# Optimization experiments

Hardware: AMD Instinct MI355X
Metric: run time of the kernel (lower is better)

Reference implementation:

```python
import jax, jax.numpy as jnp
import numpy as np

B, A, E = 8192, 56, 128          # batch, num_altas (=tgt_len), embed_dim
H, HD = 4, 16                     # num_heads, head_dim = E // H // 2
LAMBDA_INIT = 0.7
EPS = 1e-5
SCALING = HD ** -0.5


def _conv1d(x, w, b):
    # x: [N, C_in, L], w: [C_out, C_in, K], 'same' padding for K=7
    y = jax.lax.conv_general_dilated(
        x, w, window_strides=(1,), padding=[(3, 3)],
        dimension_numbers=('NCH', 'OIH', 'NCH'))
    return y + b[None, :, None]


def _layernorm(v, w, b):
    m = jnp.mean(v, axis=-1, keepdims=True)
    var = jnp.mean(jnp.square(v - m), axis=-1, keepdims=True)
    return (v - m) * jax.lax.rsqrt(var + EPS) * w + b


def setup_inputs() -> dict:
    key = jax.random.key(0)
    ks = jax.random.split(key, 12)
    return {
        'x': jax.random.normal(ks[0], (B, A, E), dtype=jnp.float32),
        'w_emb': jax.random.normal(ks[1], (A, A, 7), dtype=jnp.float32) * 0.05,
        'b_emb': jnp.zeros((A,), dtype=jnp.float32),
        'w_atlas': jax.random.normal(ks[2], (E, E, 7), dtype=jnp.float32) * 0.03,
        'b_atlas': jnp.zeros((E,), dtype=jnp.float32),
        'w_k': jax.random.normal(ks[3], (E, E), dtype=jnp.float32) * 0.08,
        'qn_w': jnp.ones((HD,), dtype=jnp.float32),
        'qn_b': jnp.zeros((HD,), dtype=jnp.float32),
        'kn_w': jnp.ones((HD,), dtype=jnp.float32),
        'kn_b': jnp.zeros((HD,), dtype=jnp.float32),
        'lambda_q1': jax.random.normal(ks[4], (HD,), dtype=jnp.float32) * 0.1,
        'lambda_k1': jax.random.normal(ks[5], (HD,), dtype=jnp.float32) * 0.1,
        'lambda_q2': jax.random.normal(ks[6], (HD,), dtype=jnp.float32) * 0.1,
        'lambda_k2': jax.random.normal(ks[7], (HD,), dtype=jnp.float32) * 0.1,
    }


def reference(x, w_emb, b_emb, w_atlas, b_atlas, w_k,
              qn_w, qn_b, kn_w, kn_b,
              lambda_q1, lambda_k1, lambda_q2, lambda_k2):
    bsz, tgt_len, embed_dim = x.shape
    # query formation: conv over atlas channels, SiLU, conv over embed channels,
    # SiLU, mean-pool over atlas positions -> [B, 1, E]
    h = jax.nn.silu(_conv1d(x, w_emb, b_emb))                  # [B, A, E]
    h = jax.nn.silu(_conv1d(h.transpose(0, 2, 1), w_atlas, b_atlas))  # [B, E, A]
    q = jnp.mean(h, axis=2)[:, None, :]                         # [B, 1, E]

    k = jnp.einsum('ble,oe->blo', x, w_k)                       # [B, A, E]

    q = q.reshape(bsz, 1, 2 * H, HD)
    k = k.reshape(bsz, tgt_len, 2 * H, HD)
    q = _layernorm(q, qn_w, qn_b) * SCALING
    k = _layernorm(k, kn_w, kn_b)

    attn = jnp.einsum('bqhe,bkhe->bhqk', q, k)                  # [B, 2H, 1, A]
    attn = jax.nn.softmax(attn, axis=-1)

    lam1 = jnp.exp(jnp.sum(lambda_q1 * lambda_k1))
    lam2 = jnp.exp(jnp.sum(lambda_q2 * lambda_k2))
    lambda_full = lam1 - lam2 + LAMBDA_INIT

    attn = attn.reshape(bsz, H, 2, 1, tgt_len)
    diff = attn[:, :, 0] - lambda_full * attn[:, :, 1]          # [B, H, 1, A]
    out = jax.nn.softmax(diff, axis=-1).mean(axis=1)            # [B, 1, A]
    return out.reshape(bsz, -1)                                 # [B, A]
```

## Files before the change

### kernel.cpp

```cpp
#include <hip/hip_runtime.h>
#include <math.h>

#define A_DIM 56
#define E_DIM 128

typedef short short8 __attribute__((ext_vector_type(8)));
typedef float floatx4 __attribute__((ext_vector_type(4)));

#define XT_HI_B 0
#define XT_LO_B 19296
#define H_HI_B  0
#define H_LO_B  16864
#define XR_HI_B 0
#define XR_LO_B 15232
#define KM_B    0
#define Q_B     33728
#define QN_B    34240
#define LG_B    34752
#define DP_B    36672
#define LAM_B   38592
#define SMEM_B  38608

#define QF   (Q_B/4)
#define QNF  (QN_B/4)
#define LGF  (LG_B/4)
#define DPF  (DP_B/4)
#define LAMF (LAM_B/4)
#define KP2  132

#define W1H 0
#define W1L 28672
#define W2H 57344
#define W2L 172032
#define WKH 286720
#define WKL 303104
#define PREP_ELEMS 159744

__device__ __forceinline__ unsigned rne16(unsigned u) {
  return (u + 0x7FFFu + ((u >> 16) & 1u)) >> 16;
}
__device__ __forceinline__ unsigned pack_hi16(unsigned u0, unsigned u1) {
  return __builtin_amdgcn_perm(u1, u0, 0x07060302u);
}
__device__ __forceinline__ float silu_f(float v) { return v / (1.f + __expf(-v)); }

__global__ void prep_weights(const float* __restrict__ w_emb,
                             const float* __restrict__ w_atlas,
                             const float* __restrict__ w_k,
                             unsigned short* __restrict__ ws) {
  int idx = blockIdx.x * 256 + threadIdx.x;
  if (idx >= PREP_ELEMS) return;
  float v; int dst_hi, dst_lo;
  if (idx < 28672) {
    int tap = idx >> 12, kc = (idx >> 11) & 1, nt = (idx >> 9) & 3;
    int lm = (idx >> 5) & 15, lkg = (idx >> 3) & 3, jj = idx & 7;
    int a = nt * 16 + lm, ci = kc * 32 + lkg * 8 + jj;
    v = (a < A_DIM && ci < A_DIM) ? w_emb[(a * A_DIM + ci) * 7 + tap] : 0.f;
    dst_hi = W1H + idx; dst_lo = W1L + idx;
  } else if (idx < 143360) {
    int j = idx - 28672;
    int tap = j >> 14, kc = (j >> 12) & 3, mt = (j >> 9) & 7;
    int lm = (j >> 5) & 15, lkg = (j >> 3) & 3, jj = j & 7;
    int eo = mt * 16 + lm, ei = kc * 32 + lkg * 8 + jj;
    v = w_atlas[(eo * E_DIM + ei) * 7 + tap];
    dst_hi = W2H + j; dst_lo = W2L + j;
  } else {
    int j = idx - 143360;
    int kc = j >> 12, mt = (j >> 9) & 7;
    int lm = (j >> 5) & 15, lkg = (j >> 3) & 3, jj = j & 7;
    int o = mt * 16 + lm, e = kc * 32 + lkg * 8 + jj;
    v = w_k[o * E_DIM + e];
    dst_hi = WKH + j; dst_lo = WKL + j;
  }
  unsigned u = __float_as_uint(v);
  unsigned hi = rne16(u);
  float lof = v - __uint_as_float(hi << 16);
  unsigned lo = rne16(__float_as_uint(lof));
  ws[dst_hi] = (unsigned short)hi;
  ws[dst_lo] = (unsigned short)lo;
}

__global__ __launch_bounds__(256, 4)
void atlas_fused(const float* __restrict__ x,
                 const unsigned short* __restrict__ ws,
                 const float* __restrict__ b_emb, const float* __restrict__ b_atlas,
                 const float* __restrict__ qn_w,  const float* __restrict__ qn_b,
                 const float* __restrict__ kn_w,  const float* __restrict__ kn_b,
                 const float* __restrict__ lq1,   const float* __restrict__ lk1,
                 const float* __restrict__ lq2,   const float* __restrict__ lk2,
                 float* __restrict__ out)
{
  __shared__ __align__(16) unsigned char smem[SMEM_B];
  float* smf = (float*)smem;
  const int t = threadIdx.x;
  const int b = blockIdx.x;
  const int lane = t & 63;
  const int w = __builtin_amdgcn_readfirstlane(t >> 6);
  const int lm = lane & 15;
  const int lkg8 = (lane >> 4) * 8;
  const int lr = (lane >> 4) * 4;

  const float* xb = x + (size_t)b * (A_DIM * E_DIM);

  {
    uint4 z4 = make_uint4(0, 0, 0, 0);
    for (int i = t; i < 352; i += 256) {
      if (i < 268) {
        int arr = i & 1, row = i >> 1;
        *(uint4*)(smem + (arr ? XT_LO_B : XT_HI_B) + row * 144 + 112) = z4;
      } else {
        int j = i - 268;
        int arr = j / 42; j -= arr * 42;
        int rowi = j / 7, c = j - rowi * 7;
        int row = (rowi < 3) ? rowi : 128 + rowi;
        *(uint4*)(smem + (arr ? XT_LO_B : XT_HI_B) + row * 144 + c * 16) = z4;
      }
    }
    if (t == 0) {
      float s1 = 0.f, s2 = 0.f;
      for (int i = 0; i < 16; ++i) { s1 += lq1[i] * lk1[i]; s2 += lq2[i] * lk2[i]; }
      smf[LAMF] = expf(s1) - expf(s2) + 0.7f;
    }
    int ab = t & 15;
    if (ab < 14) {
#pragma unroll
      for (int p = 0; p < 2; ++p) {
        int eb = (t >> 4) + 16 * p;
        floatx4 r0 = *(const floatx4*)(xb + (4 * ab + 0) * 128 + 4 * eb);
        floatx4 r1 = *(const floatx4*)(xb + (4 * ab + 1) * 128 + 4 * eb);
        floatx4 r2 = *(const floatx4*)(xb + (4 * ab + 2) * 128 + 4 * eb);
        floatx4 r3 = *(const floatx4*)(xb + (4 * ab + 3) * 128 + 4 * eb);
#pragma unroll
        for (int j2 = 0; j2 < 4; ++j2) {
          unsigned u0 = __float_as_uint(r0[j2]);
          unsigned u1 = __float_as_uint(r1[j2]);
          unsigned u2 = __float_as_uint(r2[j2]);
          unsigned u3 = __float_as_uint(r3[j2]);
          float l0 = r0[j2] - __uint_as_float(u0 & 0xFFFF0000u);
          float l1 = r1[j2] - __uint_as_float(u1 & 0xFFFF0000u);
          float l2 = r2[j2] - __uint_as_float(u2 & 0xFFFF0000u);
          float l3 = r3[j2] - __uint_as_float(u3 & 0xFFFF0000u);
          int off = (4 * eb + j2 + 3) * 144 + 8 * ab;
          *(uint2*)(smem + XT_HI_B + off) =
              make_uint2(pack_hi16(u0, u1), pack_hi16(u2, u3));
          *(uint2*)(smem + XT_LO_B + off) =
              make_uint2(pack_hi16(__float_as_uint(l0), __float_as_uint(l1)),
                         pack_hi16(__float_as_uint(l2), __float_as_uint(l3)));
        }
      }
    }
  }
  __syncthreads();

  {
    floatx4 acc[2][4];
#pragma unroll
    for (int nt = 0; nt < 4; ++nt) {
      int a = nt * 16 + lm;
      float be = (a < A_DIM) ? b_emb[a] : 0.f;
#pragma unroll
      for (int mt = 0; mt < 2; ++mt) {
        acc[mt][nt][0] = be; acc[mt][nt][1] = be;
        acc[mt][nt][2] = be; acc[mt][nt][3] = be;
      }
    }
    const unsigned short* xh = (const unsigned short*)(smem + XT_HI_B);
    const unsigned short* xl = (const unsigned short*)(smem + XT_LO_B);
#pragma unroll 1
    for (int tap = 0; tap < 7; ++tap) {
      int arow0 = (32 * w + lm + tap) * 72;
      int arow1 = arow0 + 16 * 72;
#pragma unroll
      for (int kc = 0; kc < 2; ++kc) {
        int ko = kc * 32 + lkg8;
        const unsigned short* fb = ws + ((tap * 2 + kc) * 4) * 512 + lm * 32 + lkg8;
        short8 bh0 = *(const short8*)(fb + W1H);
        short8 bh1 = *(const short8*)(fb + W1H + 512);
        short8 bh2 = *(const short8*)(fb + W1H + 1024);
        short8 bh3 = *(const short8*)(fb + W1H + 1536);
        short8 bl0 = *(const short8*)(fb + W1L);
        short8 bl1 = *(const short8*)(fb + W1L + 512);
        short8 bl2 = *(const short8*)(fb + W1L + 1024);
        short8 bl3 = *(const short8*)(fb + W1L + 1536);
        short8 ah0 = *(const short8*)(xh + arow0 + ko);
        short8 ah1 = *(const short8*)(xh + arow1 + ko);
        short8 al0 = *(const short8*)(xl + arow0 + ko);
        short8 al1 = *(const short8*)(xl + arow1 + ko);
        short8 bh[4] = {bh0, bh1, bh2, bh3};
        short8 bl[4] = {bl0, bl1, bl2, bl3};
#pragma unroll
        for (int nt = 0; nt < 4; ++nt) {
          acc[0][nt] = __builtin_amdgcn_mfma_f32_16x16x32_bf16(ah0, bh[nt], acc[0][nt], 0, 0, 0);
          acc[0][nt] = __builtin_amdgcn_mfma_f32_16x16x32_bf16(al0, bh[nt], acc[0][nt], 0, 0, 0);
          acc[0][nt] = __builtin_amdgcn_mfma_f32_16x16x32_bf16(ah0, bl[nt], acc[0][nt], 0, 0, 0);
          acc[1][nt] = __builtin_amdgcn_mfma_f32_16x16x32_bf16(ah1, bh[nt], acc[1][nt], 0, 0, 0);
          acc[1][nt] = __builtin_amdgcn_mfma_f32_16x16x32_bf16(al1, bh[nt], acc[1][nt], 0, 0, 0);
          acc[1][nt] = __builtin_amdgcn_mfma_f32_16x16x32_bf16(ah1, bl[nt], acc[1][nt], 0, 0, 0);
        }
      }
    }
    __syncthreads();
    {
      uint4 z4 = make_uint4(0, 0, 0, 0);
      for (int i = t; i < 204; i += 256) {
        int arr = i / 102, j = i - arr * 102;
        int r6 = j / 17, c = j - r6 * 17;
        int row = (r6 < 3) ? r6 : 56 + r6;
        *(uint4*)(smem + (arr ? H_LO_B : H_HI_B) + row * 272 + c * 16) = z4;
      }
    }
#pragma unroll
    for (int mt = 0; mt < 2; ++mt) {
      int e0 = 16 * (2 * w + mt) + lr;
#pragma unroll
      for (int nt = 0; nt < 4; ++nt) {
        int a = 16 * nt + lm;
        if (a < A_DIM) {
          float v0 = silu_f(acc[mt][nt][0]), v1 = silu_f(acc[mt][nt][1]);
          float v2 = silu_f(acc[mt][nt][2]), v3 = silu_f(acc[mt][nt][3]);
          unsigned u0 = __float_as_uint(v0), u1 = __float_as_uint(v1);
          unsigned u2 = __float_as_uint(v2), u3 = __float_as_uint(v3);
          float l0 = v0 - __uint_as_float(u0 & 0xFFFF0000u);
          float l1 = v1 - __uint_as_float(u1 & 0xFFFF0000u);
          float l2 = v2 - __uint_as_float(u2 & 0xFFFF0000u);
          float l3 = v3 - __uint_as_float(u3 & 0xFFFF0000u);
          int off = (a + 3) * 272 + e0 * 2;
          *(uint2*)(smem + H_HI_B + off) = make_uint2(pack_hi16(u0, u1), pack_hi16(u2, u3));
          *(uint2*)(smem + H_LO_B + off) =
              make_uint2(pack_hi16(__float_as_uint(l0), __float_as_uint(l1)),
                         pack_hi16(__float_as_uint(l2), __float_as_uint(l3)));
        }
      }
    }
  }
  __syncthreads();

  {
    floatx4 acc[2][4];
#pragma unroll
    for (int mt = 0; mt < 2; ++mt) {
      int eo0 = 16 * (2 * w + mt) + lr;
      float c0 = b_atlas[eo0], c1 = b_atlas[eo0 + 1];
      float c2 = b_atlas[eo0 + 2], c3 = b_atlas[eo0 + 3];
#pragma unroll
      for (int nt = 0; nt < 4; ++nt) {
        acc[mt][nt][0] = c0; acc[mt][nt][1] = c1;
        acc[mt][nt][2] = c2; acc[mt][nt][3] = c3;
      }
    }
    const unsigned char* hh = smem + H_HI_B;
    const unsigned char* hl = smem + H_LO_B;
#pragma unroll 1
    for (int tap = 0; tap < 7; ++tap) {
      int rofs[4];
#pragma unroll
      for (int nt = 0; nt < 4; ++nt) {
        int r = 16 * nt + lm + tap;
        rofs[nt] = ((r > 61) ? 61 : r) * 272;
      }
#pragma unroll
      for (int kc = 0; kc < 4; ++kc) {
        int kob = (kc * 32 + lkg8) * 2;
        const unsigned short* fb = ws + ((tap * 4 + kc) * 8 + 2 * w) * 512 + lm * 32 + lkg8;
        short8 ah0 = *(const short8*)(fb + W2H);
        short8 ah1 = *(const short8*)(fb + W2H + 512);
        short8 al0 = *(const short8*)(fb + W2L);
        short8 al1 = *(const short8*)(fb + W2L + 512);
        short8 bh[4], bl[4];
#pragma unroll
        for (int nt = 0; nt < 4; ++nt) {
          bh[nt] = *(const short8*)(hh + rofs[nt] + kob);
          bl[nt] = *(const short8*)(hl + rofs[nt] + kob);
        }
#pragma unroll
        for (int nt = 0; nt < 4; ++nt) {
          acc[0][nt] = __builtin_amdgcn_mfma_f32_16x16x32_bf16(ah0, bh[nt], acc[0][nt], 0, 0, 0);
          acc[0][nt] = __builtin_amdgcn_mfma_f32_16x16x32_bf16(al0, bh[nt], acc[0][nt], 0, 0, 0);
          acc[0][nt] = __builtin_amdgcn_mfma_f32_16x16x32_bf16(ah0, bl[nt], acc[0][nt], 0, 0, 0);
          acc[1][nt] = __builtin_amdgcn_mfma_f32_16x16x32_bf16(ah1, bh[nt], acc[1][nt], 0, 0, 0);
          acc[1][nt] = __builtin_amdgcn_mfma_f32_16x16x32_bf16(al1, bh[nt], acc[1][nt], 0, 0, 0);
          acc[1][nt] = __builtin_amdgcn_mfma_f32_16x16x32_bf16(ah1, bl[nt], acc[1][nt], 0, 0, 0);
        }
      }
    }
#pragma unroll
    for (int mt = 0; mt < 2; ++mt) {
#pragma unroll
      for (int r = 0; r < 4; ++r) {
        float s = 0.f;
#pragma unroll
        for (int nt = 0; nt < 4; ++nt) {
          float v = silu_f(acc[mt][nt][r]);
          int a = 16 * nt + lm;
          s += (a < A_DIM) ? v : 0.f;
        }
        s += __shfl_xor(s, 1, 64);
        s += __shfl_xor(s, 2, 64);
        s += __shfl_xor(s, 4, 64);
        s += __shfl_xor(s, 8, 64);
        if (lm == 0) {
          int eo = 16 * (2 * w + mt) + lr + r;
          smf[QF + eo] = s * (1.f / 56.f);
        }
      }
    }
  }
  __syncthreads();

  if (t < 128) {
    float v = smf[QF + t];
    float s = v;
#pragma unroll
    for (int m = 1; m < 16; m <<= 1) s += __shfl_xor(s, m, 64);
    float mean = s * (1.f / 16.f);
    float d = v - mean;
    float s2 = d * d;
#pragma unroll
    for (int m = 1; m < 16; m <<= 1) s2 += __shfl_xor(s2, m, 64);
    float var = s2 * (1.f / 16.f);
    int dd = t & 15;
    float qn = d * rsqrtf(var + 1e-5f) * qn_w[dd] + qn_b[dd];
    smf[QNF + t] = qn * 0.25f;
  }
  for (int i = t; i < 1792; i += 256) {
    int a = i >> 5, e4 = i & 31;
    float4 v = *(const float4*)(xb + a * 128 + e4 * 4);
    unsigned u0 = __float_as_uint(v.x), u1 = __float_as_uint(v.y);
    unsigned u2 = __float_as_uint(v.z), u3 = __float_as_uint(v.w);
    float l0 = v.x - __uint_as_float(u0 & 0xFFFF0000u);
    float l1 = v.y - __uint_as_float(u1 & 0xFFFF0000u);
    float l2 = v.z - __uint_as_float(u2 & 0xFFFF0000u);
    float l3 = v.w - __uint_as_float(u3 & 0xFFFF0000u);
    int off = a * 272 + e4 * 8;
    *(uint2*)(smem + XR_HI_B + off) = make_uint2(pack_hi16(u0, u1), pack_hi16(u2, u3));
    *(uint2*)(smem + XR_LO_B + off) =
        make_uint2(pack_hi16(__float_as_uint(l0), __float_as_uint(l1)),
                   pack_hi16(__float_as_uint(l2), __float_as_uint(l3)));
  }
  __syncthreads();

  {
    floatx4 acc[2][4];
#pragma unroll
    for (int mt = 0; mt < 2; ++mt)
#pragma unroll
      for (int nt = 0; nt < 4; ++nt) {
        acc[mt][nt][0] = 0.f; acc[mt][nt][1] = 0.f;
        acc[mt][nt][2] = 0.f; acc[mt][nt][3] = 0.f;
      }
    const unsigned char* xrh = smem + XR_HI_B;
    const unsigned char* xrl = smem + XR_LO_B;
    int rofs[4];
#pragma unroll
    for (int nt = 0; nt < 4; ++nt) {
      int a = 16 * nt + lm;
      rofs[nt] = ((a > 55) ? 55 : a) * 272;
    }
#pragma unroll 1
    for (int kc = 0; kc < 4; ++kc) {
      int kob = (kc * 32 + lkg8) * 2;
      const unsigned short* fb = ws + (kc * 8 + 2 * w) * 512 + lm * 32 + lkg8;
      short8 ah0 = *(const short8*)(fb + WKH);
      short8 ah1 = *(const short8*)(fb + WKH + 512);
      short8 al0 = *(const short8*)(fb + WKL);
      short8 al1 = *(const short8*)(fb + WKL + 512);
      short8 bh[4], bl[4];
#pragma unroll
      for (int nt = 0; nt < 4; ++nt) {
        bh[nt] = *(const short8*)(xrh + rofs[nt] + kob);
        bl[nt] = *(const short8*)(xrl + rofs[nt] + kob);
      }
#pragma unroll
      for (int nt = 0; nt < 4; ++nt) {
        acc[0][nt] = __builtin_amdgcn_mfma_f32_16x16x32_bf16(ah0, bh[nt], acc[0][nt], 0, 0, 0);
        acc[0][nt] = __builtin_amdgcn_mfma_f32_16x16x32_bf16(al0, bh[nt], acc[0][nt], 0, 0, 0);
        acc[0][nt] = __builtin_amdgcn_mfma_f32_16x16x32_bf16(ah0, bl[nt], acc[0][nt], 0, 0, 0);
        acc[1][nt] = __builtin_amdgcn_mfma_f32_16x16x32_bf16(ah1, bh[nt], acc[1][nt], 0, 0, 0);
        acc[1][nt] = __builtin_amdgcn_mfma_f32_16x16x32_bf16(al1, bh[nt], acc[1][nt], 0, 0, 0);
        acc[1][nt] = __builtin_amdgcn_mfma_f32_16x16x32_bf16(ah1, bl[nt], acc[1][nt], 0, 0, 0);
      }
    }
    __syncthreads();
#pragma unroll
    for (int mt = 0; mt < 2; ++mt) {
      int o0 = 16 * (2 * w + mt) + lr;
#pragma unroll
      for (int nt = 0; nt < 4; ++nt) {
        int a = 16 * nt + lm;
        if (a < A_DIM)
          *(floatx4*)&smf[(KM_B / 4) + a * KP2 + o0] = acc[mt][nt];
      }
    }
  }
  __syncthreads();

  for (int r = 0; r < 2; ++r) {
    int task = t + r * 256;
    if (task < A_DIM * 8) {
      int a = task >> 3, h2 = task & 7;
      float kv[16];
      float s = 0.f;
#pragma unroll
      for (int d = 0; d < 16; ++d) { kv[d] = smf[(KM_B / 4) + a * KP2 + h2 * 16 + d]; s += kv[d]; }
      float mean = s * (1.f / 16.f);
      float s2 = 0.f;
#pragma unroll
      for (int d = 0; d < 16; ++d) { float dd = kv[d] - mean; s2 += dd * dd; }
      float rs = rsqrtf(s2 * (1.f / 16.f) + 1e-5f);
      float logit = 0.f;
#pragma unroll
      for (int d = 0; d < 16; ++d) {
        float kn = (kv[d] - mean) * rs * kn_w[d] + kn_b[d];
        logit += smf[QNF + h2 * 16 + d] * kn;
      }
      smf[LGF + h2 * 60 + a] = logit;
    }
  }
  __syncthreads();

  {
    int g = t >> 5;
    int l = t & 31;
    float v0 = smf[LGF + g * 60 + l];
    bool has1 = (l < A_DIM - 32);
    float v1 = has1 ? smf[LGF + g * 60 + 32 + l] : -1e30f;
    float m = fmaxf(v0, v1);
#pragma unroll
    for (int s = 1; s < 32; s <<= 1) m = fmaxf(m, __shfl_xor(m, s, 64));
    float e0 = expf(v0 - m);
    float e1 = has1 ? expf(v1 - m) : 0.f;
    float ssum = e0 + e1;
#pragma unroll
    for (int s = 1; s < 32; s <<= 1) ssum += __shfl_xor(ssum, s, 64);
    float inv = 1.f / ssum;
    smf[LGF + g * 60 + l] = e0 * inv;
    if (has1) smf[LGF + g * 60 + 32 + l] = e1 * inv;
  }
  __syncthreads();

  {
    int h = t >> 6;
    int a = t & 63;
    float lam = smf[LAMF];
    float dlog = -1e30f;
    if (a < A_DIM) {
      float p0 = smf[LGF + (2 * h) * 60 + a];
      float p1 = smf[LGF + (2 * h + 1) * 60 + a];
      dlog = p0 - lam * p1;
    }
    float m = dlog;
#pragma unroll
    for (int s = 1; s < 64; s <<= 1) m = fmaxf(m, __shfl_xor(m, s, 64));
    float e = (a < A_DIM) ? expf(dlog - m) : 0.f;
    float ss = e;
#pragma unroll
    for (int s = 1; s < 64; s <<= 1) ss += __shfl_xor(ss, s, 64);
    if (a < A_DIM) smf[DPF + h * 60 + a] = e / ss;
  }
  __syncthreads();

  if (t < A_DIM) {
    float r = 0.25f * (smf[DPF + t] + smf[DPF + 60 + t] +
                       smf[DPF + 120 + t] + smf[DPF + 180 + t]);
    out[(size_t)b * A_DIM + t] = r;
  }
}

extern "C" void kernel_launch(void* const* d_in, const int* in_sizes, int n_in,
                              void* d_out, int out_size, void* d_ws, size_t ws_size,
                              hipStream_t stream) {
  const float* x       = (const float*)d_in[0];
  const float* w_emb   = (const float*)d_in[1];
  const float* b_emb   = (const float*)d_in[2];
  const float* w_atlas = (const float*)d_in[3];
  const float* b_atlas = (const float*)d_in[4];
  const float* w_k     = (const float*)d_in[5];
  const float* qn_w    = (const float*)d_in[6];
  const float* qn_b    = (const float*)d_in[7];
  const float* kn_w    = (const float*)d_in[8];
  const float* kn_b    = (const float*)d_in[9];
  const float* lq1     = (const float*)d_in[10];
  const float* lk1     = (const float*)d_in[11];
  const float* lq2     = (const float*)d_in[12];
  const float* lk2     = (const float*)d_in[13];
  float* out = (float*)d_out;
  unsigned short* ws = (unsigned short*)d_ws;

  prep_weights<<<dim3((PREP_ELEMS + 255) / 256), dim3(256), 0, stream>>>(
      w_emb, w_atlas, w_k, ws);

  const int Bn = in_sizes[0] / (A_DIM * E_DIM);
  atlas_fused<<<dim3(Bn), dim3(256), 0, stream>>>(
      x, ws, b_emb, b_atlas, qn_w, qn_b, kn_w, kn_b,
      lq1, lk1, lq2, lk2, out);
}
```

Measured before the change: 806.1 us.

## Split-K the second conv GEMM across wave pairs with LDS reduction

The embed-channel conv stage is repartitioned. Previously each wave computed 2 output tiles over the full reduction. Now waves pair up: each wave computes 4 output tiles over half of the K chunks, so every activation fragment loaded from LDS feeds twice as many MFMAs. The two partial sums are combined through an LDS buffer that reuses the H region, and the bias, SiLU and mean-pool are applied afterwards. In exchange the accumulator registers double and the stage gains two extra barriers plus LDS store/load traffic for the reduction, which could cut occupancy.

```diff
diff --git a/kernel.cpp b/kernel.cpp
--- a/kernel.cpp
+++ b/kernel.cpp
@@ -11,6 +11,7 @@
 #define XT_LO_B 19296
 #define H_HI_B  0
 #define H_LO_B  16864
+#define RB_B    0
 #define XR_HI_B 0
 #define XR_LO_B 15232
 #define KM_B    0
@@ -236,18 +237,15 @@
   __syncthreads();
 
   {
-    floatx4 acc[2][4];
-#pragma unroll
-    for (int mt = 0; mt < 2; ++mt) {
-      int eo0 = 16 * (2 * w + mt) + lr;
-      float c0 = b_atlas[eo0], c1 = b_atlas[eo0 + 1];
-      float c2 = b_atlas[eo0 + 2], c3 = b_atlas[eo0 + 3];
-#pragma unroll
-      for (int nt = 0; nt < 4; ++nt) {
-        acc[mt][nt][0] = c0; acc[mt][nt][1] = c1;
-        acc[mt][nt][2] = c2; acc[mt][nt][3] = c3;
-      }
-    }
+    const int g = w >> 1, p = w & 1;
+    floatx4 acc[4][4];
+#pragma unroll
+    for (int mt = 0; mt < 4; ++mt)
+#pragma unroll
+      for (int nt = 0; nt < 4; ++nt) {
+        acc[mt][nt][0] = 0.f; acc[mt][nt][1] = 0.f;
+        acc[mt][nt][2] = 0.f; acc[mt][nt][3] = 0.f;
+      }
     const unsigned char* hh = smem + H_HI_B;
     const unsigned char* hl = smem + H_LO_B;
 #pragma unroll 1
@@ -259,48 +257,67 @@
         rofs[nt] = ((r > 61) ? 61 : r) * 272;
       }
 #pragma unroll
-      for (int kc = 0; kc < 4; ++kc) {
+      for (int kc2 = 0; kc2 < 2; ++kc2) {
+        int kc = 2 * g + kc2;
         int kob = (kc * 32 + lkg8) * 2;
-        const unsigned short* fb = ws + ((tap * 4 + kc) * 8 + 2 * w) * 512 + lm * 32 + lkg8;
-        short8 ah0 = *(const short8*)(fb + W2H);
-        short8 ah1 = *(const short8*)(fb + W2H + 512);
-        short8 al0 = *(const short8*)(fb + W2L);
-        short8 al1 = *(const short8*)(fb + W2L + 512);
         short8 bh[4], bl[4];
 #pragma unroll
         for (int nt = 0; nt < 4; ++nt) {
           bh[nt] = *(const short8*)(hh + rofs[nt] + kob);
           bl[nt] = *(const short8*)(hl + rofs[nt] + kob);
         }
+        const unsigned short* fb0 =
+            ws + ((tap * 4 + kc) * 8 + 4 * p) * 512 + lm * 32 + lkg8;
+#pragma unroll
+        for (int mt = 0; mt < 4; ++mt) {
+          short8 ah = *(const short8*)(fb0 + W2H + mt * 512);
+          short8 al = *(const short8*)(fb0 + W2L + mt * 512);
+#pragma unroll
+          for (int nt = 0; nt < 4; ++nt) {
+            acc[mt][nt] = __builtin_amdgcn_mfma_f32_16x16x32_bf16(ah, bh[nt], acc[mt][nt], 0, 0, 0);
+            acc[mt][nt] = __builtin_amdgcn_mfma_f32_16x16x32_bf16(al, bh[nt], acc[mt][nt], 0, 0, 0);
+            acc[mt][nt] = __builtin_amdgcn_mfma_f32_16x16x32_bf16(ah, bl[nt], acc[mt][nt], 0, 0, 0);
+          }
+        }
+      }
+    }
+    __syncthreads();
+    float* rb = (float*)(smem + RB_B + p * 16384);
+    if (g == 1) {
+#pragma unroll
+      for (int mt = 0; mt < 4; ++mt)
+#pragma unroll
+        for (int nt = 0; nt < 4; ++nt)
+          *(floatx4*)(rb + ((mt * 4 + nt) * 64 + lane) * 4) = acc[mt][nt];
+    }
+    __syncthreads();
+    if (g == 0) {
+#pragma unroll
+      for (int mt = 0; mt < 4; ++mt) {
+        int eo0 = 64 * p + 16 * mt + lr;
+        floatx4 bias4;
+        bias4[0] = b_atlas[eo0];     bias4[1] = b_atlas[eo0 + 1];
+        bias4[2] = b_atlas[eo0 + 2]; bias4[3] = b_atlas[eo0 + 3];
+        floatx4 tot[4];
 #pragma unroll
         for (int nt = 0; nt < 4; ++nt) {
-          acc[0][nt] = __builtin_amdgcn_mfma_f32_16x16x32_bf16(ah0, bh[nt], acc[0][nt], 0, 0, 0);
-          acc[0][nt] = __builtin_amdgcn_mfma_f32_16x16x32_bf16(al0, bh[nt], acc[0][nt], 0, 0, 0);
-          acc[0][nt] = __builtin_amdgcn_mfma_f32_16x16x32_bf16(ah0, bl[nt], acc[0][nt], 0, 0, 0);
-          acc[1][nt] = __builtin_amdgcn_mfma_f32_16x16x32_bf16(ah1, bh[nt], acc[1][nt], 0, 0, 0);
-          acc[1][nt] = __builtin_amdgcn_mfma_f32_16x16x32_bf16(al1, bh[nt], acc[1][nt], 0, 0, 0);
-          acc[1][nt] = __builtin_amdgcn_mfma_f32_16x16x32_bf16(ah1, bl[nt], acc[1][nt], 0, 0, 0);
-        }
-      }
-    }
-#pragma unroll
-    for (int mt = 0; mt < 2; ++mt) {
-#pragma unroll
-      for (int r = 0; r < 4; ++r) {
-        float s = 0.f;
-#pragma unroll
-        for (int nt = 0; nt < 4; ++nt) {
-          float v = silu_f(acc[mt][nt][r]);
-          int a = 16 * nt + lm;
-          s += (a < A_DIM) ? v : 0.f;
-        }
-        s += __shfl_xor(s, 1, 64);
-        s += __shfl_xor(s, 2, 64);
-        s += __shfl_xor(s, 4, 64);
-        s += __shfl_xor(s, 8, 64);
-        if (lm == 0) {
-          int eo = 16 * (2 * w + mt) + lr + r;
-          smf[QF + eo] = s * (1.f / 56.f);
+          floatx4 part = *(const floatx4*)(rb + ((mt * 4 + nt) * 64 + lane) * 4);
+          tot[nt] = acc[mt][nt] + part + bias4;
+        }
+#pragma unroll
+        for (int r = 0; r < 4; ++r) {
+          float s = 0.f;
+#pragma unroll
+          for (int nt = 0; nt < 4; ++nt) {
+            float v = silu_f(tot[nt][r]);
+            int a = 16 * nt + lm;
+            s += (a < A_DIM) ? v : 0.f;
+          }
+          s += __shfl_xor(s, 1, 64);
+          s += __shfl_xor(s, 2, 64);
+          s += __shfl_xor(s, 4, 64);
+          s += __shfl_xor(s, 8, 64);
+          if (lm == 0) smf[QF + eo0 + r] = s * (1.f / 56.f);
         }
       }
     }
```

After: 819.0 us. Within noise of the previous version (+1.6%).
